# Performance work log

Hardware: AMD Instinct MI355X
Metric: run time of the kernel (lower is better)

Reference implementation:

```python
import jax, jax.numpy as jnp
import numpy as np

EMBED_DIM = 1024
NUM_HEADS = 16
HEAD_DIM = EMBED_DIM // NUM_HEADS
SCALING = (1.0 / HEAD_DIM) ** 0.5


def setup_inputs() -> dict:
    key = jax.random.key(0)
    ks = jax.random.split(key, 9)
    d = EMBED_DIM
    return {
        "hidden_states": jax.random.normal(ks[0], (4, 2048, d), dtype=jnp.float32),
        "q_w": jax.random.normal(ks[1], (d, d), dtype=jnp.float32) * 0.02,
        "q_b": jax.random.normal(ks[2], (d,), dtype=jnp.float32) * 0.02,
        "k_w": jax.random.normal(ks[3], (d, d), dtype=jnp.float32) * 0.02,
        "k_b": jax.random.normal(ks[4], (d,), dtype=jnp.float32) * 0.02,
        "v_w": jax.random.normal(ks[5], (d, d), dtype=jnp.float32) * 0.02,
        "v_b": jax.random.normal(ks[6], (d,), dtype=jnp.float32) * 0.02,
        "out_w": jax.random.normal(ks[7], (d, d), dtype=jnp.float32) * 0.02,
        "out_b": jax.random.normal(ks[8], (d,), dtype=jnp.float32) * 0.02,
    }


def _shape(x, bsz, seq, nh, hd):
    # [B, T, E] -> [B, H, T, Hd]
    return x.reshape(bsz, seq, nh, hd).transpose(0, 2, 1, 3)


def reference(hidden_states, q_w, q_b, k_w, k_b, v_w, v_b, out_w, out_b):
    bsz, tgt_len, _ = hidden_states.shape
    # torch Linear: y = x @ W.T + b; query scaled by sqrt(1/head_dim)
    q = (hidden_states @ q_w.T + q_b) * SCALING
    k = hidden_states @ k_w.T + k_b
    v = hidden_states @ v_w.T + v_b
    q = _shape(q, bsz, tgt_len, NUM_HEADS, HEAD_DIM)
    k = _shape(k, bsz, tgt_len, NUM_HEADS, HEAD_DIM)
    v = _shape(v, bsz, tgt_len, NUM_HEADS, HEAD_DIM)
    # [B, H, T, S]
    attn_weights = jnp.einsum("bhtd,bhsd->bhts", q, k)
    attn_weights = jax.nn.softmax(attn_weights, axis=-1)
    # [B, H, T, Hd] -> [B, T, E]
    attn_output = jnp.einsum("bhts,bhsd->bhtd", attn_weights, v)
    attn_output = attn_output.transpose(0, 2, 1, 3).reshape(bsz, tgt_len, EMBED_DIM)
    return attn_output @ out_w.T + out_b
```

## Files before the change

kernel.cpp:

```cpp
#include <hip/hip_runtime.h>
#include <hip/hip_bf16.h>
#include <cstdint>
#include <math.h>

typedef uint16_t u16;
typedef __attribute__((ext_vector_type(8))) short short8;
typedef __attribute__((ext_vector_type(2))) float floatx2;
typedef __attribute__((ext_vector_type(4))) float floatx4;
typedef __attribute__((ext_vector_type(16))) float floatx16;

__device__ __forceinline__ float bf2f(u16 u) {
  return __uint_as_float(((uint32_t)u) << 16);
}
__device__ __forceinline__ u16 f2bf(float f) {
  uint32_t u = __float_as_uint(f);
  u += 0x7FFF + ((u >> 16) & 1);
  return (u16)(u >> 16);
}

#if __has_builtin(__builtin_amdgcn_exp2f)
#define EXP2(x) __builtin_amdgcn_exp2f(x)
#else
#define EXP2(x) exp2f(x)
#endif

__device__ __forceinline__ void glds16(const void* g, void* l) {
  __builtin_amdgcn_global_load_lds(
      (const __attribute__((address_space(1))) void*)g,
      (__attribute__((address_space(3))) void*)l, 16, 0, 0);
}

__device__ __forceinline__ bool detect_fp32(const u16* __restrict__ hs) {
  int big = 0;
#pragma unroll
  for (int i = 0; i < 128; ++i) {
    const int e = (hs[i] >> 7) & 0xFF;
    big += (e >= 140);
  }
  return big > 0;
}

__device__ __forceinline__ void conv_blk(
    const void* __restrict__ src, u16* __restrict__ dst, int i, bool f32)
{
  if (f32) {
    const float4 v = ((const float4*)src)[i];
    ushort4 d;
    d.x = f2bf(v.x); d.y = f2bf(v.y); d.z = f2bf(v.z); d.w = f2bf(v.w);
    ((ushort4*)dst)[i] = d;
  } else {
    ((ushort4*)dst)[i] = ((const ushort4*)src)[i];
  }
}

__global__ __launch_bounds__(256) void convert_all(
    const void* __restrict__ hs, const void* __restrict__ qw,
    const void* __restrict__ kw, const void* __restrict__ vw,
    const void* __restrict__ ow, const void* __restrict__ qb,
    const void* __restrict__ kb, const void* __restrict__ vb,
    const void* __restrict__ ob,
    u16* __restrict__ d_hs, u16* __restrict__ d_qw, u16* __restrict__ d_kw,
    u16* __restrict__ d_vw, u16* __restrict__ d_ow, u16* __restrict__ d_qb,
    u16* __restrict__ d_kb, u16* __restrict__ d_vb, u16* __restrict__ d_ob)
{
  const bool f32 = detect_fp32((const u16*)hs);
  const int bid = blockIdx.x;
  const int tid = threadIdx.x;
  if (bid < 2048) {
#pragma unroll
    for (int k = 0; k < 4; ++k)
      conv_blk(hs, d_hs, bid * 1024 + k * 256 + tid, f32);
  } else if (bid < 2048 + 1024) {
    const int w = (bid - 2048) >> 8;
    const int base = ((bid - 2048) & 255) * 1024;
    const void* s = (w == 0) ? qw : (w == 1) ? kw : (w == 2) ? vw : ow;
    u16* d        = (w == 0) ? d_qw : (w == 1) ? d_kw : (w == 2) ? d_vw : d_ow;
#pragma unroll
    for (int k = 0; k < 4; ++k)
      conv_blk(s, d, base + k * 256 + tid, f32);
  } else {
    const int w = bid - 3072;
    const void* s = (w == 0) ? qb : (w == 1) ? kb : (w == 2) ? vb : ob;
    u16* d        = (w == 0) ? d_qb : (w == 1) ? d_kb : (w == 2) ? d_vb : d_ob;
    conv_blk(s, d, tid, f32);
  }
}

template <int MODE>
__device__ __forceinline__ void gemm_body(
    const u16* __restrict__ A, const u16* __restrict__ W,
    const u16* __restrict__ bias, void* __restrict__ vout,
    float scale, u16* As, u16* Bs, int bx, int by, bool f32out)
{
  constexpr int KD = 1024;
  const int tid  = threadIdx.x;
  const int lane = tid & 63;
  const int l15  = lane & 15;
  const int quad = lane >> 4;
  const int wid  = tid >> 6;
  const int bm = by * 128, bn = bx * 128;
  const int wm = (wid >> 1) * 64, wn = (wid & 1) * 64;

  floatx4 acc[4][4];
#pragma unroll
  for (int i = 0; i < 4; ++i)
#pragma unroll
    for (int j = 0; j < 4; ++j)
#pragma unroll
      for (int r = 0; r < 4; ++r) acc[i][j][r] = 0.0f;

  const int c0 = tid, c1 = tid + 256;
  const u16* Ag0 = A + (size_t)(bm + (c0 >> 2)) * KD + (c0 & 3) * 8;
  const u16* Ag1 = A + (size_t)(bm + (c1 >> 2)) * KD + (c1 & 3) * 8;
  const u16* Wg0 = W + (size_t)(bn + (c0 >> 2)) * KD + (c0 & 3) * 8;
  const u16* Wg1 = W + (size_t)(bn + (c1 >> 2)) * KD + (c1 & 3) * 8;
  u16* As0 = As + c0 * 8;  u16* As1 = As + c1 * 8;
  u16* Bs0 = Bs + c0 * 8;  u16* Bs1 = Bs + c1 * 8;

  for (int kt = 0; kt < KD / 64; ++kt) {
    const int ko = kt * 64;
    glds16(Ag0 + ko, As0);
    glds16(Ag1 + ko, As1);
    glds16(Wg0 + ko, Bs0);
    glds16(Wg1 + ko, Bs1);
    glds16(Ag0 + ko + 32, As0 + 4096);
    glds16(Ag1 + ko + 32, As1 + 4096);
    glds16(Wg0 + ko + 32, Bs0 + 4096);
    glds16(Wg1 + ko + 32, Bs1 + 4096);
    __syncthreads();
#pragma unroll
    for (int h = 0; h < 2; ++h) {
      const u16* Ah = As + h * 4096;
      const u16* Bh = Bs + h * 4096;
      short8 af[4], bf[4];
#pragma unroll
      for (int mb = 0; mb < 4; ++mb)
        af[mb] = *(const short8*)&Ah[(wm + mb * 16 + l15) * 32 + quad * 8];
#pragma unroll
      for (int nb = 0; nb < 4; ++nb)
        bf[nb] = *(const short8*)&Bh[(wn + nb * 16 + l15) * 32 + quad * 8];
#pragma unroll
      for (int mb = 0; mb < 4; ++mb)
#pragma unroll
        for (int nb = 0; nb < 4; ++nb) {
          if (MODE == 2)
            acc[mb][nb] = __builtin_amdgcn_mfma_f32_16x16x32_bf16(
                bf[nb], af[mb], acc[mb][nb], 0, 0, 0);
          else
            acc[mb][nb] = __builtin_amdgcn_mfma_f32_16x16x32_bf16(
                af[mb], bf[nb], acc[mb][nb], 0, 0, 0);
        }
    }
    __syncthreads();
  }

  if (MODE == 2) {
#pragma unroll
    for (int nb = 0; nb < 4; ++nb)
#pragma unroll
      for (int r = 0; r < 4; ++r) {
        const int wrow = bn + wn + nb * 16 + quad * 4 + r;
        const float bv = bf2f(bias[wrow]);
        const int h = wrow >> 6, d = wrow & 63;
        u16* out = (u16*)vout;
#pragma unroll
        for (int mb = 0; mb < 4; ++mb) {
          const int tcol = bm + wm + mb * 16 + l15;
          const int b = tcol >> 11, t = tcol & 2047;
          out[((size_t)(b * 16 + h) * 64 + d) * 2048 + t] =
              f2bf((acc[mb][nb][r] + bv) * scale);
        }
      }
  } else {
    float bias_v[4];
#pragma unroll
    for (int nb = 0; nb < 4; ++nb) bias_v[nb] = bf2f(bias[bn + wn + nb * 16 + l15]);
#pragma unroll
    for (int mb = 0; mb < 4; ++mb)
#pragma unroll
      for (int nb = 0; nb < 4; ++nb)
#pragma unroll
        for (int r = 0; r < 4; ++r) {
          const int row = bm + wm + mb * 16 + quad * 4 + r;
          const int col = bn + wn + nb * 16 + l15;
          const float v = (acc[mb][nb][r] + bias_v[nb]) * scale;
          if (MODE == 0) {
            if (f32out) ((float*)vout)[(size_t)row * 1024 + col] = v;
            else        ((u16*)vout)[(size_t)row * 1024 + col] = f2bf(v);
          } else {
            const int b = row >> 11, t = row & 2047;
            const int h = col >> 6, d = col & 63;
            ((u16*)vout)[(((size_t)(b * 16 + h)) * 2048 + t) * 64 + d] = f2bf(v);
          }
        }
  }
}

__global__ __launch_bounds__(256, 3) void gemm_qkv(
    const u16* __restrict__ A,
    const u16* __restrict__ Wq, const u16* __restrict__ Wk, const u16* __restrict__ Wv,
    const u16* __restrict__ bq, const u16* __restrict__ bk, const u16* __restrict__ bv,
    u16* __restrict__ Oq, u16* __restrict__ Ok, u16* __restrict__ Ov)
{
  __shared__ u16 As[2 * 128 * 32];
  __shared__ u16 Bs[2 * 128 * 32];
  const int lid = blockIdx.x + 8 * blockIdx.y + 512 * blockIdx.z;
  const int w   = (lid & 7) * 192 + (lid >> 3);
  const int bx  = w & 7;
  const int by  = (w >> 3) & 63;
  const int z   = w >> 9;
  if (z < 2) {
    const u16* Wt   = z ? Wk : Wq;
    const u16* bias = z ? bk : bq;
    u16* out        = z ? Ok : Oq;
    const float scale = z ? 1.0f : 0.125f;
    gemm_body<1>(A, Wt, bias, out, scale, As, Bs, bx, by, false);
  } else {
    gemm_body<2>(A, Wv, bv, Ov, 1.0f, As, Bs, bx, by, false);
  }
}

__global__ __launch_bounds__(256, 3) void gemm_out_proj(
    const u16* __restrict__ A, const u16* __restrict__ W,
    const u16* __restrict__ bias, void* __restrict__ out,
    const u16* __restrict__ probe)
{
  __shared__ u16 As[2 * 128 * 32];
  __shared__ u16 Bs[2 * 128 * 32];
  const bool f32 = detect_fp32(probe);
  const int lid = blockIdx.x + 8 * blockIdx.y;
  const int w   = (lid & 7) * 64 + (lid >> 3);
  const int bx  = w & 7;
  const int by  = w >> 3;
  gemm_body<0>(A, W, bias, out, 1.0f, As, Bs, bx, by, f32);
}

__global__ __launch_bounds__(256, 2) void attn_fused(
    const u16* __restrict__ Q, const u16* __restrict__ K,
    const u16* __restrict__ VT, u16* __restrict__ O)
{
  constexpr int T = 2048, D = 64;
  constexpr int KS = 72;
  __shared__ u16 Ks[2][64 * KS];
  __shared__ u16 Vts[2][64 * KS];
  __shared__ float Linv[128];

  const int tid  = threadIdx.x;
  const int lane = tid & 63;
  const int l31  = lane & 31;
  const int half = lane >> 5;
  const int wid  = tid >> 6;
  const int lid = blockIdx.x + 16 * blockIdx.y;
  const int wkid = (lid & 7) * 128 + (lid >> 3);
  const int qt = wkid & 15;
  const int bh = wkid >> 4;
  const int q0w = wid * 32;

  const u16* Qb = Q + (size_t)bh * T * D + (size_t)qt * 128 * D;
  const u16* Kb = K + (size_t)bh * T * D;
  const u16* Vb = VT + (size_t)bh * D * T;

  const int c0r = tid >> 3,        c0o = (tid & 7) * 8;
  const int c1r = (tid + 256) >> 3, c1o = ((tid + 256) & 7) * 8;

  short8 qf[4];
#pragma unroll
  for (int kk = 0; kk < 4; ++kk)
    qf[kk] = *(const short8*)&Qb[(q0w + l31) * D + kk * 16 + half * 8];

  floatx16 o_acc[2];
#pragma unroll
  for (int dt = 0; dt < 2; ++dt)
#pragma unroll
    for (int i = 0; i < 16; ++i) o_acc[dt][i] = 0.0f;
  floatx2 l01 = {0.0f, 0.0f}, l23 = {0.0f, 0.0f};

  const floatx2 L2E2 = {1.4426950408889634f, 1.4426950408889634f};

  short8 krg0, krg1, vrg0, vrg1;
  krg0 = *(const short8*)&Kb[(size_t)c0r * D + c0o];
  krg1 = *(const short8*)&Kb[(size_t)c1r * D + c1o];
  vrg0 = *(const short8*)&Vb[(size_t)c0r * T + c0o];
  vrg1 = *(const short8*)&Vb[(size_t)c1r * T + c1o];

#pragma unroll 1
  for (int kt = 0; kt < T / 64; ++kt) {
    const int cur = kt & 1;
    *(short8*)&Ks[cur][c0r * KS + c0o] = krg0;
    *(short8*)&Ks[cur][c1r * KS + c1o] = krg1;
    *(short8*)&Vts[cur][c0r * KS + c0o] = vrg0;
    *(short8*)&Vts[cur][c1r * KS + c1o] = vrg1;
    __syncthreads();
    if (kt + 1 < T / 64) {
      const u16* Kt = Kb + (size_t)(kt + 1) * 64 * D;
      krg0 = *(const short8*)&Kt[(size_t)c0r * D + c0o];
      krg1 = *(const short8*)&Kt[(size_t)c1r * D + c1o];
      vrg0 = *(const short8*)&Vb[(size_t)c0r * T + (kt + 1) * 64 + c0o];
      vrg1 = *(const short8*)&Vb[(size_t)c1r * T + (kt + 1) * 64 + c1o];
    }

#pragma unroll
    for (int t = 0; t < 2; ++t) {
      floatx16 s;
#pragma unroll
      for (int i = 0; i < 16; ++i) s[i] = 0.0f;
      __builtin_amdgcn_s_setprio(1);
#pragma unroll
      for (int kk = 0; kk < 4; ++kk) {
        const short8 kf =
            *(const short8*)&Ks[cur][(t * 32 + l31) * KS + kk * 16 + half * 8];
        s = __builtin_amdgcn_mfma_f32_32x32x16_bf16(kf, qf[kk], s, 0, 0, 0);
      }
      __builtin_amdgcn_s_setprio(0);
      uint32_t e[4][2];
#pragma unroll
      for (int g = 0; g < 4; ++g) {
        const floatx2 s01 = {s[4 * g + 0], s[4 * g + 1]};
        const floatx2 s23 = {s[4 * g + 2], s[4 * g + 3]};
        floatx2 t01, t23;
        asm("v_pk_mul_f32 %0, %1, %2" : "=v"(t01) : "v"(s01), "v"(L2E2));
        asm("v_pk_mul_f32 %0, %1, %2" : "=v"(t23) : "v"(s23), "v"(L2E2));
        floatx2 p01, p23;
        p01.x = EXP2(fminf(t01.x, 44.f));
        p01.y = EXP2(fminf(t01.y, 44.f));
        p23.x = EXP2(fminf(t23.x, 44.f));
        p23.y = EXP2(fminf(t23.y, 44.f));
        asm("v_pk_add_f32 %0, %0, %1" : "+v"(l01) : "v"(p01));
        asm("v_pk_add_f32 %0, %0, %1" : "+v"(l23) : "v"(p23));
        asm("v_cvt_pk_bf16_f32 %0, %1, %2" : "=v"(e[g][0]) : "v"(p01.x), "v"(p01.y));
        asm("v_cvt_pk_bf16_f32 %0, %1, %2" : "=v"(e[g][1]) : "v"(p23.x), "v"(p23.y));
      }
#pragma unroll
      for (int c = 0; c < 2; ++c) {
        uint32_t a0 = e[2 * c][0], b0 = e[2 * c + 1][0];
        uint32_t a1 = e[2 * c][1], b1 = e[2 * c + 1][1];
        asm("v_permlane32_swap_b32 %0, %1" : "+v"(a0), "+v"(b0));
        asm("v_permlane32_swap_b32 %0, %1" : "+v"(a1), "+v"(b1));
        union { uint32_t u[4]; short8 v; } pu;
        pu.u[0] = a0; pu.u[1] = a1; pu.u[2] = b0; pu.u[3] = b1;
        const short8 pf = pu.v;
        const int kkp = 2 * t + c;
        const short8 vf0 =
            *(const short8*)&Vts[cur][l31 * KS + kkp * 16 + half * 8];
        const short8 vf1 =
            *(const short8*)&Vts[cur][(32 + l31) * KS + kkp * 16 + half * 8];
        __builtin_amdgcn_s_setprio(1);
        o_acc[0] = __builtin_amdgcn_mfma_f32_32x32x16_bf16(pf, vf0, o_acc[0], 0, 0, 0);
        o_acc[1] = __builtin_amdgcn_mfma_f32_32x32x16_bf16(pf, vf1, o_acc[1], 0, 0, 0);
        __builtin_amdgcn_s_setprio(0);
      }
    }
  }

  const float l_acc = (l01.x + l01.y) + (l23.x + l23.y);
  uint32_t lu0 = __float_as_uint(l_acc), lu1 = lu0;
  asm("v_permlane32_swap_b32 %0, %1" : "+v"(lu0), "+v"(lu1));
  const float l_full = l_acc + __uint_as_float(half ? lu0 : lu1);
  __syncthreads();
  Linv[q0w + l31] = 1.0f / l_full;

  const int b = bh >> 4, h = bh & 15;
  u16* Ob = O + ((size_t)b * 2048 + (size_t)qt * 128) * 1024 + h * 64;
  float invs[16];
  __syncthreads();
#pragma unroll
  for (int i = 0; i < 16; ++i)
    invs[i] = Linv[q0w + (i & 3) + 8 * (i >> 2) + 4 * half];
#pragma unroll
  for (int dt = 0; dt < 2; ++dt)
#pragma unroll
    for (int i = 0; i < 16; ++i) {
      const int qrow = q0w + (i & 3) + 8 * (i >> 2) + 4 * half;
      Ob[(size_t)qrow * 1024 + dt * 32 + l31] = f2bf((float)o_acc[dt][i] * invs[i]);
    }
}

extern "C" void kernel_launch(void* const* d_in, const int* in_sizes, int n_in,
                              void* d_out, int out_size, void* d_ws, size_t ws_size,
                              hipStream_t stream) {
  const u16* hs_probe = (const u16*)d_in[0];

  const size_t TE = (size_t)4 * 2048 * 1024;
  const size_t WE = (size_t)1024 * 1024;
  u16* hsB = (u16*)d_ws;
  u16* Qb  = hsB + TE;
  u16* Kb  = Qb + TE;
  u16* Vb  = Kb + TE;
  u16* Ob  = Vb + TE;
  u16* qwB = Ob + TE;
  u16* kwB = qwB + WE;
  u16* vwB = kwB + WE;
  u16* owB = vwB + WE;
  u16* qbB = owB + WE;
  u16* kbB = qbB + 1024;
  u16* vbB = kbB + 1024;
  u16* obB = vbB + 1024;

  dim3 bb(256);
  convert_all<<<dim3(3076), bb, 0, stream>>>(
      d_in[0], d_in[1], d_in[3], d_in[5], d_in[7],
      d_in[2], d_in[4], d_in[6], d_in[8],
      hsB, qwB, kwB, vwB, owB, qbB, kbB, vbB, obB);

  gemm_qkv<<<dim3(8, 64, 3), bb, 0, stream>>>(
      hsB, qwB, kwB, vwB, qbB, kbB, vbB, Qb, Kb, Vb);
  attn_fused<<<dim3(16, 64), bb, 0, stream>>>(Qb, Kb, Vb, Ob);
  gemm_out_proj<<<dim3(8, 64), bb, 0, stream>>>(Ob, owB, obB, d_out, hs_probe);
}
```

Before: 288.0 us.

## Enlarge GEMM block tile to 256x128 with 512-thread blocks

The QKV and output-projection GEMMs move from 128x128 tiles with 256 threads to 256x128 tiles with 512 threads (8 waves). Each B (weight) tile loaded into LDS is now reused across twice as many rows. This cuts global and LDS traffic per output element and halves the number of blocks. The block-index swizzle and grid sizes are updated to match. In exchange, LDS per block grows and only 768 (QKV) or 256 (out-proj) blocks are launched. That could hurt load balance and occupancy on a CU-rich GPU.

```diff
diff --git a/kernel.cpp b/kernel.cpp
--- a/kernel.cpp
+++ b/kernel.cpp
@@ -98,7 +98,7 @@
   const int l15  = lane & 15;
   const int quad = lane >> 4;
   const int wid  = tid >> 6;
-  const int bm = by * 128, bn = bx * 128;
+  const int bm = by * 256, bn = bx * 128;
   const int wm = (wid >> 1) * 64, wn = (wid & 1) * 64;
 
   floatx4 acc[4][4];
@@ -109,28 +109,24 @@
 #pragma unroll
       for (int r = 0; r < 4; ++r) acc[i][j][r] = 0.0f;
 
-  const int c0 = tid, c1 = tid + 256;
-  const u16* Ag0 = A + (size_t)(bm + (c0 >> 2)) * KD + (c0 & 3) * 8;
-  const u16* Ag1 = A + (size_t)(bm + (c1 >> 2)) * KD + (c1 & 3) * 8;
-  const u16* Wg0 = W + (size_t)(bn + (c0 >> 2)) * KD + (c0 & 3) * 8;
-  const u16* Wg1 = W + (size_t)(bn + (c1 >> 2)) * KD + (c1 & 3) * 8;
-  u16* As0 = As + c0 * 8;  u16* As1 = As + c1 * 8;
-  u16* Bs0 = Bs + c0 * 8;  u16* Bs1 = Bs + c1 * 8;
+  const u16* Ag0 = A + (size_t)(bm + (tid >> 2)) * KD + (tid & 3) * 8;
+  const u16* Ag1 = Ag0 + (size_t)128 * KD;
+  const u16* Wg0 = W + (size_t)(bn + (tid >> 2)) * KD + (tid & 3) * 8;
+  u16* AsD = As + tid * 8;
+  u16* BsD = Bs + tid * 8;
 
   for (int kt = 0; kt < KD / 64; ++kt) {
     const int ko = kt * 64;
-    glds16(Ag0 + ko, As0);
-    glds16(Ag1 + ko, As1);
-    glds16(Wg0 + ko, Bs0);
-    glds16(Wg1 + ko, Bs1);
-    glds16(Ag0 + ko + 32, As0 + 4096);
-    glds16(Ag1 + ko + 32, As1 + 4096);
-    glds16(Wg0 + ko + 32, Bs0 + 4096);
-    glds16(Wg1 + ko + 32, Bs1 + 4096);
+    glds16(Ag0 + ko,      AsD);
+    glds16(Ag1 + ko,      AsD + 4096);
+    glds16(Wg0 + ko,      BsD);
+    glds16(Ag0 + ko + 32, AsD + 8192);
+    glds16(Ag1 + ko + 32, AsD + 8192 + 4096);
+    glds16(Wg0 + ko + 32, BsD + 4096);
     __syncthreads();
 #pragma unroll
     for (int h = 0; h < 2; ++h) {
-      const u16* Ah = As + h * 4096;
+      const u16* Ah = As + h * 8192;
       const u16* Bh = Bs + h * 4096;
       short8 af[4], bf[4];
 #pragma unroll
@@ -196,19 +192,19 @@
   }
 }
 
-__global__ __launch_bounds__(256, 3) void gemm_qkv(
+__global__ __launch_bounds__(512, 2) void gemm_qkv(
     const u16* __restrict__ A,
     const u16* __restrict__ Wq, const u16* __restrict__ Wk, const u16* __restrict__ Wv,
     const u16* __restrict__ bq, const u16* __restrict__ bk, const u16* __restrict__ bv,
     u16* __restrict__ Oq, u16* __restrict__ Ok, u16* __restrict__ Ov)
 {
-  __shared__ u16 As[2 * 128 * 32];
+  __shared__ u16 As[2 * 256 * 32];
   __shared__ u16 Bs[2 * 128 * 32];
-  const int lid = blockIdx.x + 8 * blockIdx.y + 512 * blockIdx.z;
-  const int w   = (lid & 7) * 192 + (lid >> 3);
+  const int lid = blockIdx.x + 8 * blockIdx.y + 256 * blockIdx.z;
+  const int w   = (lid & 7) * 96 + (lid >> 3);
   const int bx  = w & 7;
-  const int by  = (w >> 3) & 63;
-  const int z   = w >> 9;
+  const int by  = (w >> 3) & 31;
+  const int z   = w >> 8;
   if (z < 2) {
     const u16* Wt   = z ? Wk : Wq;
     const u16* bias = z ? bk : bq;
@@ -220,16 +216,16 @@
   }
 }
 
-__global__ __launch_bounds__(256, 3) void gemm_out_proj(
+__global__ __launch_bounds__(512, 2) void gemm_out_proj(
     const u16* __restrict__ A, const u16* __restrict__ W,
     const u16* __restrict__ bias, void* __restrict__ out,
     const u16* __restrict__ probe)
 {
-  __shared__ u16 As[2 * 128 * 32];
+  __shared__ u16 As[2 * 256 * 32];
   __shared__ u16 Bs[2 * 128 * 32];
   const bool f32 = detect_fp32(probe);
   const int lid = blockIdx.x + 8 * blockIdx.y;
-  const int w   = (lid & 7) * 64 + (lid >> 3);
+  const int w   = (lid & 7) * 32 + (lid >> 3);
   const int bx  = w & 7;
   const int by  = w >> 3;
   gemm_body<0>(A, W, bias, out, 1.0f, As, Bs, bx, by, f32);
@@ -397,13 +393,14 @@
   u16* obB = vbB + 1024;
 
   dim3 bb(256);
+  dim3 gb(512);
   convert_all<<<dim3(3076), bb, 0, stream>>>(
       d_in[0], d_in[1], d_in[3], d_in[5], d_in[7],
       d_in[2], d_in[4], d_in[6], d_in[8],
       hsB, qwB, kwB, vwB, owB, qbB, kbB, vbB, obB);
 
-  gemm_qkv<<<dim3(8, 64, 3), bb, 0, stream>>>(
+  gemm_qkv<<<dim3(8, 32, 3), gb, 0, stream>>>(
       hsB, qwB, kwB, vwB, qbB, kbB, vbB, Qb, Kb, Vb);
   attn_fused<<<dim3(16, 64), bb, 0, stream>>>(Qb, Kb, Vb, Ob);
-  gemm_out_proj<<<dim3(8, 64), bb, 0, stream>>>(Ob, owB, obB, d_out, hs_probe);
-}
+  gemm_out_proj<<<dim3(8, 32), gb, 0, stream>>>(Ob, owB, obB, d_out, hs_probe);
+}
```

Measured after the change: 287.6 us. Within noise of the previous version (-0.1%).
